# Performance work log

Measured on AMD Instinct MI355X. Metric: run time of the kernel, lower is better.

Reference implementation:

```python
import jax, jax.numpy as jnp
import numpy as np

FEATURE_HEIGHT = 50
FEATURE_WIDTH = 50


def setup_inputs() -> dict:
    key = jax.random.key(0)
    k1, k2, k3 = jax.random.split(key, 3)
    bs, K, H, D = 16, FEATURE_HEIGHT * FEATURE_WIDTH, 8, 32
    Q, L, P = 2000, 1, 4
    value = jax.random.normal(k1, (bs, K, H, D), dtype=jnp.float32)
    value_spatial_shapes = jnp.array([[FEATURE_HEIGHT, FEATURE_WIDTH]], dtype=jnp.int64)
    sampling_locations = jax.random.uniform(k2, (bs, Q, H, L, P, 2), dtype=jnp.float32)
    attention_weights = jax.random.uniform(k3, (bs, Q, H, L, P), dtype=jnp.float32)
    return {
        "value": value,
        "value_spatial_shapes": value_spatial_shapes,
        "sampling_locations": sampling_locations,
        "attention_weights": attention_weights,
    }


def _bilinear_sample(img, grid):
    """torch.F.grid_sample(mode='bilinear', padding_mode='zeros', align_corners=False).

    img:  (N, D, h, w)
    grid: (N, Q, P, 2), last dim (x, y) in [-1, 1]
    returns (N, D, Q, P)
    """
    N, D, h, w = img.shape
    # unnormalize (align_corners=False)
    x = (grid[..., 0] + 1.0) * (w * 0.5) - 0.5  # (N, Q, P)
    y = (grid[..., 1] + 1.0) * (h * 0.5) - 0.5
    x0 = jnp.floor(x)
    y0 = jnp.floor(y)
    x1 = x0 + 1.0
    y1 = y0 + 1.0
    wx1 = x - x0
    wx0 = 1.0 - wx1
    wy1 = y - y0
    wy0 = 1.0 - wy1

    img_flat = img.reshape(N, D, h * w)

    def corner(ix, iy, wgt):
        valid = ((ix >= 0) & (ix < w) & (iy >= 0) & (iy < h)).astype(img.dtype)
        ixc = jnp.clip(ix, 0, w - 1).astype(jnp.int32)
        iyc = jnp.clip(iy, 0, h - 1).astype(jnp.int32)
        idx = (iyc * w + ixc).reshape(N, -1)  # (N, Q*P)
        vals = jnp.take_along_axis(img_flat, idx[:, None, :], axis=2)  # (N, D, Q*P)
        vals = vals.reshape(N, D, *ix.shape[1:])  # (N, D, Q, P)
        return vals * (wgt * valid)[:, None]

    out = corner(x0, y0, wx0 * wy0)
    out = out + corner(x1, y0, wx1 * wy0)
    out = out + corner(x0, y1, wx0 * wy1)
    out = out + corner(x1, y1, wx1 * wy1)
    return out


def reference(value, value_spatial_shapes, sampling_locations, attention_weights):
    bs, K, H, D = value.shape
    _, Q, _, L, P, _ = sampling_locations.shape
    h, w = FEATURE_HEIGHT, FEATURE_WIDTH

    sampling_grids = 2.0 * sampling_locations - 1.0  # (bs, Q, H, L, P, 2)
    # value -> (bs*H, D, h, w)
    v = value.reshape(bs, K, H * D).transpose(0, 2, 1).reshape(bs * H, D, h, w)
    # level 0 grid -> (bs*H, Q, P, 2)
    g = jnp.transpose(sampling_grids[:, :, :, 0], (0, 2, 1, 3, 4)).reshape(bs * H, Q, P, 2)
    sampled = _bilinear_sample(v, g)  # (bs*H, D, Q, P)
    # attention weights -> (bs*H, 1, Q, L*P)
    aw = jnp.transpose(attention_weights, (0, 2, 1, 3, 4)).reshape(bs * H, 1, Q, L * P)
    out = (sampled * aw).sum(-1)  # (bs*H, D, Q)
    out = out.reshape(bs, H * D, Q).transpose(0, 2, 1)  # (bs, Q, H*D)
    return out
```

## Files before the change

### kernel.cpp

```cpp
#include <hip/hip_runtime.h>


#define FH 50
#define FW 50
#define KK (FH * FW)
#define NH 8
#define ND 32
#define NQ 2000
#define NP 4
#define TPB 1024
#define QHB 1000

typedef float f32x4 __attribute__((ext_vector_type(4)));
typedef _Float16 f16x8 __attribute__((ext_vector_type(8)));
typedef _Float16 f16x4 __attribute__((ext_vector_type(4)));

__global__ __launch_bounds__(TPB)
__attribute__((amdgpu_waves_per_eu(4, 4)))
void deform_attn_kernel(
    const float* __restrict__ value,
    const float* __restrict__ loc,
    const float* __restrict__ attw,
    float* __restrict__ out)
{
    const int id = blockIdx.x;
    const int xcd = id & 7;
    const int slot = id >> 3;
    const int qh  = slot & 1;
    const int h   = (slot >> 1) & 7;
    const int b   = ((slot >> 4) << 3) | xcd;

    __shared__ _Float16 ldsH[KK * ND];

    const int t = threadIdx.x;

#pragma unroll
    for (int i = 0; i < 20; ++i) {
        const int u = i * TPB + t;
        if (u < KK * 8) {
            const int k = u >> 3;
            const int c0 = (u & 7) * 4;
            const f32x4 v4 = *(const f32x4*)(
                value + ((size_t)(b * KK + k) * NH + h) * ND + c0);
            f16x4 h4;
            h4[0] = (_Float16)v4.x;  h4[1] = (_Float16)v4.y;
            h4[2] = (_Float16)v4.z;  h4[3] = (_Float16)v4.w;
            const int j  = (u & 7) >> 1;
            const int js = j ^ ((k >> 1) & 3);
            *(f16x4*)((char*)ldsH + k * 64 + js * 16 + (u & 1) * 8) = h4;
        }
    }
    __syncthreads();

    const f32x4* __restrict__ lp = (const f32x4*)loc;
    const f32x4* __restrict__ ap = (const f32x4*)attw;
    const char*  __restrict__ lbase = (const char*)ldsH;

#pragma unroll 1
    for (int pass = 0; pass < 2; ++pass) {
        const int unit = pass * TPB + t;
        if (unit < 2 * QHB) {
            const int q   = qh * QHB + (unit >> 1);
            const int chh = unit & 1;
            const int cb  = chh << 5;

            const int gid = (b * NQ + q) * NH + h;
            const f32x4 l0 = lp[(size_t)gid * 2 + 0];
            const f32x4 l1 = lp[(size_t)gid * 2 + 1];
            const f32x4 a4 = ap[gid];

            float acc[16];
#pragma unroll
            for (int c = 0; c < 16; ++c) acc[c] = 0.f;

            const float pxx[NP] = {l0.x, l0.z, l1.x, l1.z};
            const float pyy[NP] = {l0.y, l0.w, l1.y, l1.w};
            const float awp[NP] = {a4.x, a4.y, a4.z, a4.w};

#pragma unroll
            for (int p = 0; p < NP; ++p) {
                const float fx = pxx[p] * (float)FW - 0.5f;
                const float fy = pyy[p] * (float)FH - 0.5f;
                const float x0f = floorf(fx);
                const float y0f = floorf(fy);
                const int x0 = (int)x0f, y0 = (int)y0f;
                const int x1 = x0 + 1, y1 = y0 + 1;
                const float wx1 = fx - x0f, wx0 = 1.f - wx1;
                const float wy1 = fy - y0f, wy0 = 1.f - wy1;

                const bool vx0 = (x0 >= 0) & (x0 < FW);
                const bool vx1 = (x1 >= 0) & (x1 < FW);
                const bool vy0 = (y0 >= 0) & (y0 < FH);
                const bool vy1 = (y1 >= 0) & (y1 < FH);

                const int cx0 = min(max(x0, 0), FW - 1);
                const int cx1 = min(max(x1, 0), FW - 1);
                const int cy0 = min(max(y0, 0), FH - 1);
                const int cy1 = min(max(y1, 0), FH - 1);

                const int kc[4] = {cy0 * FW + cx0, cy0 * FW + cx1,
                                   cy1 * FW + cx0, cy1 * FW + cx1};
                const float wc[4] = {
                    ((vx0 & vy0) ? (wx0 * wy0) : 0.f) * awp[p],
                    ((vx1 & vy0) ? (wx1 * wy0) : 0.f) * awp[p],
                    ((vx0 & vy1) ? (wx0 * wy1) : 0.f) * awp[p],
                    ((vx1 & vy1) ? (wx1 * wy1) : 0.f) * awp[p]};

#pragma unroll
                for (int cr = 0; cr < 4; ++cr) {
                    const int k = kc[cr];
                    const float w = wc[cr];
                    const int A = ((k << 6) + (((k >> 1) & 3) << 4)) ^ cb;
                    const f16x8 v0 = *(const f16x8*)(lbase + A);
                    const f16x8 v1 = *(const f16x8*)(lbase + (A ^ 16));
#pragma unroll
                    for (int c = 0; c < 8; ++c) {
                        acc[c]     += w * (float)v0[c];
                        acc[8 + c] += w * (float)v1[c];
                    }
                }
            }

            float* o = out + (size_t)(b * NQ + q) * (NH * ND)
                           + h * ND + chh * 16;
#pragma unroll
            for (int j = 0; j < 4; ++j) {
                f32x4 s = {acc[j * 4 + 0], acc[j * 4 + 1],
                           acc[j * 4 + 2], acc[j * 4 + 3]};
                *(f32x4*)(o + j * 4) = s;
            }
        }
    }
}

extern "C" void kernel_launch(void* const* d_in, const int* in_sizes, int n_in,
                              void* d_out, int out_size, void* d_ws, size_t ws_size,
                              hipStream_t stream) {
    const float* value = (const float*)d_in[0];
    const float* loc  = (const float*)d_in[2];
    const float* attw = (const float*)d_in[3];
    float* out = (float*)d_out;

    const int blocks = 2 * 16 * 8;
    deform_attn_kernel<<<blocks, TPB, 0, stream>>>(value, loc, attw, out);
}
```

Measured before the change: 117.9 us.

## Split channel halves across blocks to halve LDS and double occupancy

Each block now stages only 16 of the 32 channels for one (batch, head) in LDS, which halves shared memory to 80KB. The block covers all 2000 queries instead of half, and the per-query channel split moves into the block index. The LDS swizzle is redesigned for 32-byte rows, and waves_per_eu rises from 4 to 8 so two blocks can be resident per CU. The trade-off is that sampling locations and weights are now read twice (once per channel half) and each thread recomputes the bilinear coordinates.

```diff
diff --git a/kernel.cpp b/kernel.cpp
--- a/kernel.cpp
+++ b/kernel.cpp
@@ -9,14 +9,17 @@
 #define NQ 2000
 #define NP 4
 #define TPB 1024
-#define QHB 1000
 
 typedef float f32x4 __attribute__((ext_vector_type(4)));
 typedef _Float16 f16x8 __attribute__((ext_vector_type(8)));
 typedef _Float16 f16x4 __attribute__((ext_vector_type(4)));
 
+__device__ __forceinline__ int chunk_addr(int k, int j) {
+    return ((k >> 2) << 7) + (((((k & 3) << 1) | j) ^ ((k >> 2) & 7)) << 4);
+}
+
 __global__ __launch_bounds__(TPB)
-__attribute__((amdgpu_waves_per_eu(4, 4)))
+__attribute__((amdgpu_waves_per_eu(8, 8)))
 void deform_attn_kernel(
     const float* __restrict__ value,
     const float* __restrict__ loc,
@@ -26,44 +29,41 @@
     const int id = blockIdx.x;
     const int xcd = id & 7;
     const int slot = id >> 3;
-    const int qh  = slot & 1;
+    const int bhi = slot & 1;
     const int h   = (slot >> 1) & 7;
-    const int b   = ((slot >> 4) << 3) | xcd;
+    const int chh = (slot >> 4) & 1;
+    const int b   = (bhi << 3) | xcd;
 
-    __shared__ _Float16 ldsH[KK * ND];
+    __shared__ _Float16 ldsH[KK * 16];
 
     const int t = threadIdx.x;
 
+    const f32x4* __restrict__ lp = (const f32x4*)loc;
+    const f32x4* __restrict__ ap = (const f32x4*)attw;
+
 #pragma unroll
-    for (int i = 0; i < 20; ++i) {
+    for (int i = 0; i < 10; ++i) {
         const int u = i * TPB + t;
-        if (u < KK * 8) {
-            const int k = u >> 3;
-            const int c0 = (u & 7) * 4;
+        if (u < KK * 4) {
+            const int k = u >> 2;
+            const int cq = u & 3;
             const f32x4 v4 = *(const f32x4*)(
-                value + ((size_t)(b * KK + k) * NH + h) * ND + c0);
+                value + ((size_t)(b * KK + k) * NH + h) * ND
+                      + chh * 16 + cq * 4);
             f16x4 h4;
             h4[0] = (_Float16)v4.x;  h4[1] = (_Float16)v4.y;
             h4[2] = (_Float16)v4.z;  h4[3] = (_Float16)v4.w;
-            const int j  = (u & 7) >> 1;
-            const int js = j ^ ((k >> 1) & 3);
-            *(f16x4*)((char*)ldsH + k * 64 + js * 16 + (u & 1) * 8) = h4;
+            *(f16x4*)((char*)ldsH + chunk_addr(k, cq >> 1) + (cq & 1) * 8) = h4;
         }
     }
     __syncthreads();
 
-    const f32x4* __restrict__ lp = (const f32x4*)loc;
-    const f32x4* __restrict__ ap = (const f32x4*)attw;
-    const char*  __restrict__ lbase = (const char*)ldsH;
+    const char* __restrict__ lbase = (const char*)ldsH;
 
 #pragma unroll 1
     for (int pass = 0; pass < 2; ++pass) {
-        const int unit = pass * TPB + t;
-        if (unit < 2 * QHB) {
-            const int q   = qh * QHB + (unit >> 1);
-            const int chh = unit & 1;
-            const int cb  = chh << 5;
-
+        const int q = pass * TPB + t;
+        if (q < NQ) {
             const int gid = (b * NQ + q) * NH + h;
             const f32x4 l0 = lp[(size_t)gid * 2 + 0];
             const f32x4 l1 = lp[(size_t)gid * 2 + 1];
@@ -110,9 +110,8 @@
                 for (int cr = 0; cr < 4; ++cr) {
                     const int k = kc[cr];
                     const float w = wc[cr];
-                    const int A = ((k << 6) + (((k >> 1) & 3) << 4)) ^ cb;
-                    const f16x8 v0 = *(const f16x8*)(lbase + A);
-                    const f16x8 v1 = *(const f16x8*)(lbase + (A ^ 16));
+                    const f16x8 v0 = *(const f16x8*)(lbase + chunk_addr(k, 0));
+                    const f16x8 v1 = *(const f16x8*)(lbase + chunk_addr(k, 1));
 #pragma unroll
                     for (int c = 0; c < 8; ++c) {
                         acc[c]     += w * (float)v0[c];
```

New measurement: 222.6 us. 1.89x slower.
